# Kernel optimization log

Hardware: AMD Instinct MI355X
Metric: run time of the kernel (lower is better)

## Reference

```python
import jax, jax.numpy as jnp
import numpy as np

T, H, F, E, K = 1024, 2048, 1024, 8, 2  # tokens, hidden, intermediate, experts, top_k
RENORMALIZE = True


def setup_inputs() -> dict:
    key = jax.random.key(0)
    k1, k2, k3, k4, k5 = jax.random.split(key, 5)
    hidden_states = jax.random.normal(k1, (T, H), dtype=jnp.float32)
    router_logits = jax.random.normal(k2, (T, E), dtype=jnp.float32)
    w1 = jax.random.normal(k3, (E, H, F), dtype=jnp.float32) * 0.02  # gate proj
    w3 = jax.random.normal(k4, (E, H, F), dtype=jnp.float32) * 0.02  # up proj
    w2 = jax.random.normal(k5, (E, F, H), dtype=jnp.float32) * 0.02  # down proj
    return {"hidden_states": hidden_states, "router_logits": router_logits,
            "w1": w1, "w3": w3, "w2": w2}


def _moe_forward(x, router_logits, w1, w3, w2):
    # Top-K routing: softmax over all experts, select top-k, optional renormalize.
    probs = jax.nn.softmax(router_logits, axis=-1)            # [T, E]
    topk_vals, topk_ids = jax.lax.top_k(probs, K)             # [T, K]
    if RENORMALIZE:
        topk_vals = topk_vals / jnp.sum(topk_vals, axis=-1, keepdims=True)
    # Dense combine weights: zero for non-selected experts.   [T, E]
    tok_idx = jnp.arange(x.shape[0])[:, None]
    combine = jnp.zeros(probs.shape, dtype=x.dtype).at[tok_idx, topk_ids].set(topk_vals)
    # Expert SwiGLU FFN computed per expert over all tokens, masked-combined.
    g = jnp.einsum('th,ehf->etf', x, w1)                      # gate  [E, T, F]
    u = jnp.einsum('th,ehf->etf', x, w3)                      # up    [E, T, F]
    a = jax.nn.silu(g) * u                                    # silu activation
    y = jnp.einsum('etf,efh->eth', a, w2)                     # down  [E, T, H]
    out = jnp.einsum('eth,te->th', y, combine)                # weighted combine
    return out


def reference(hidden_states, router_logits, w1, w3, w2):
    return _moe_forward(hidden_states, router_logits, w1, w3, w2)
```

## Files before the change

kernel.cpp:

```cpp
#include <hip/hip_runtime.h>
#include <cstdint>
#include <cstddef>

#define T_TOK 1024
#define H_DIM 2048
#define F_DIM 1024
#define E_EXP 8
#define BM 64
#define BK 64
#define MAX_TILES 40
#define ROWCAP 2560

#define I_NTILES 25
#define I_TILE_E 32
#define I_TILE_R0 80
#define I_ROWTOK 4224
#define I_ROWW   6784
#define B_XB     37888
#define B_AWS    (B_XB + T_TOK*H_DIM*2)
#define B_W1T    (B_AWS + ROWCAP*F_DIM*2)
#define B_W3T    (B_W1T + E_EXP*F_DIM*H_DIM*2)
#define B_W2T    (B_W3T + E_EXP*F_DIM*H_DIM*2)

typedef __bf16 bf16x8 __attribute__((ext_vector_type(8)));
typedef float  f32x4  __attribute__((ext_vector_type(4)));

#define MFMA(a,b,c) __builtin_amdgcn_mfma_f32_16x16x32_bf16(a,b,c,0,0,0)

__device__ __forceinline__ void gload16(const void* g, void* l) {
  __builtin_amdgcn_global_load_lds(
      (const __attribute__((address_space(1))) void*)g,
      (__attribute__((address_space(3))) void*)l, 16, 0, 0);
}

__global__ __launch_bounds__(1024) void k_route(const float* __restrict__ logits,
                                                int* __restrict__ ws_i) {
  __shared__ int cnt[E_EXP], cur[E_EXP], offs_s[E_EXP];
  const int t = threadIdx.x;
  float* ws_f = (float*)ws_i;
  if (t < E_EXP) { cnt[t] = 0; cur[t] = 0; }
  __syncthreads();
  float l[E_EXP];
#pragma unroll
  for (int e = 0; e < E_EXP; ++e) l[e] = logits[t * E_EXP + e];
  int b0 = 0; float v0 = l[0];
#pragma unroll
  for (int e = 1; e < E_EXP; ++e) if (l[e] > v0) { v0 = l[e]; b0 = e; }
  int b1 = -1; float v1 = -3.4e38f;
#pragma unroll
  for (int e = 0; e < E_EXP; ++e) if (e != b0 && l[e] > v1) { v1 = l[e]; b1 = e; }
  float w0 = 1.f / (1.f + __expf(v1 - v0));
  float w1 = 1.f - w0;
  atomicAdd(&cnt[b0], 1);
  atomicAdd(&cnt[b1], 1);
  __syncthreads();
  if (t == 0) {
    int off = 0, nt = 0;
    for (int e = 0; e < E_EXP; ++e) {
      offs_s[e] = off;
      int ntile = (cnt[e] + BM - 1) / BM;
      for (int i = 0; i < ntile; ++i) {
        ws_i[I_TILE_E + nt] = e;
        ws_i[I_TILE_R0 + nt] = off + i * BM;
        ++nt;
      }
      off += ntile * BM;
    }
    ws_i[I_NTILES] = nt;
  }
  for (int i = t; i < ROWCAP; i += 1024) ws_i[I_ROWTOK + i] = -1;
  __syncthreads();
  {
    int p = atomicAdd(&cur[b0], 1);
    int s = offs_s[b0] + p;
    ws_i[I_ROWTOK + s] = t;
    ws_f[I_ROWW + s] = w0;
  }
  {
    int p = atomicAdd(&cur[b1], 1);
    int s = offs_s[b1] + p;
    ws_i[I_ROWTOK + s] = t;
    ws_f[I_ROWW + s] = w1;
  }
}

__global__ __launch_bounds__(256) void k_cvt(const float* __restrict__ x,
                                             __bf16* __restrict__ xb) {
  long i = (long)(blockIdx.x * 256 + threadIdx.x) * 8;
  float4 a = *(const float4*)(x + i);
  float4 b = *(const float4*)(x + i + 4);
  bf16x8 v;
  v[0] = (__bf16)a.x; v[1] = (__bf16)a.y; v[2] = (__bf16)a.z; v[3] = (__bf16)a.w;
  v[4] = (__bf16)b.x; v[5] = (__bf16)b.y; v[6] = (__bf16)b.z; v[7] = (__bf16)b.w;
  *(bf16x8*)(xb + i) = v;
}

__global__ __launch_bounds__(256) void k_cvtW(const float* __restrict__ w1,
                                              const float* __restrict__ w3,
                                              const float* __restrict__ w2,
                                              __bf16* __restrict__ w1t,
                                              __bf16* __restrict__ w3t,
                                              __bf16* __restrict__ w2t) {
  __shared__ __bf16 tr[64][66];
  const int z = blockIdx.z;
  const float* src; __bf16* dst; int R, C;
  if (z < 8)       { src = w1 + (size_t)z * H_DIM * F_DIM;        dst = w1t + (size_t)z * F_DIM * H_DIM;        R = H_DIM; C = F_DIM; }
  else if (z < 16) { src = w3 + (size_t)(z - 8) * H_DIM * F_DIM;  dst = w3t + (size_t)(z - 8) * F_DIM * H_DIM;  R = H_DIM; C = F_DIM; }
  else             { src = w2 + (size_t)(z - 16) * F_DIM * H_DIM; dst = w2t + (size_t)(z - 16) * H_DIM * F_DIM; R = F_DIM; C = H_DIM; }
  const int ti = blockIdx.x * 16 + blockIdx.y;
  const int nC = C >> 6;
  const int r0 = (ti / nC) * 64, c0 = (ti % nC) * 64;
  const float* s = src + (size_t)r0 * C + c0;
  __bf16* d = dst + (size_t)c0 * R + r0;
  const int t = threadIdx.x;
  const int lr = t >> 4, lc = (t & 15) * 4;
#pragma unroll
  for (int i = 0; i < 4; ++i) {
    int r = lr + i * 16;
    float4 f = *(const float4*)(s + (size_t)r * C + lc);
    tr[lc + 0][r] = (__bf16)f.x;
    tr[lc + 1][r] = (__bf16)f.y;
    tr[lc + 2][r] = (__bf16)f.z;
    tr[lc + 3][r] = (__bf16)f.w;
  }
  __syncthreads();
  const int oc = t >> 2, ok = (t & 3) * 16;
  *(bf16x8*)(d + (size_t)oc * R + ok)     = *(const bf16x8*)&tr[oc][ok];
  *(bf16x8*)(d + (size_t)oc * R + ok + 8) = *(const bf16x8*)&tr[oc][ok + 8];
}

__global__ __launch_bounds__(256) void k_gemm1(const __bf16* __restrict__ xb,
                                               const __bf16* __restrict__ w1t,
                                               const __bf16* __restrict__ w3t,
                                               const int* __restrict__ ws_i,
                                               __bf16* __restrict__ aws) {
  __shared__ __bf16 sm[2][3 * 4096];
  __shared__ int s_tok[BM];
  const int p = blockIdx.x;
  const int lg = (p & 7) * 80 + (p >> 3);
  const int tile = lg % MAX_TILES;
  const int n0 = (lg / MAX_TILES) * 64;
  if (tile >= ws_i[I_NTILES]) return;
  const int e  = ws_i[I_TILE_E + tile];
  const int r0 = ws_i[I_TILE_R0 + tile];
  const int tid = threadIdx.x, lane = tid & 63, wid = tid >> 6;
  const int wm = wid >> 1, wn = wid & 1;
  const int l15 = lane & 15, l4 = lane >> 4;
  if (tid < BM) {
    int tk = ws_i[I_ROWTOK + r0 + tid];
    s_tok[tid] = tk < 0 ? 0 : tk;
  }
  __syncthreads();
  const int rj0 = wid * 16 + (lane >> 3);
  const int rj1 = rj0 + 8;
  const int ks = ((lane & 7) ^ (lane >> 3)) * 8;
  const __bf16* gA0 = xb + (size_t)s_tok[rj0] * H_DIM + ks;
  const __bf16* gA1 = xb + (size_t)s_tok[rj1] * H_DIM + ks;
  const __bf16* w1e = w1t + (size_t)e * F_DIM * H_DIM;
  const __bf16* w3e = w3t + (size_t)e * F_DIM * H_DIM;
  const __bf16* gB1_0 = w1e + (size_t)(n0 + rj0) * H_DIM + ks;
  const __bf16* gB1_1 = w1e + (size_t)(n0 + rj1) * H_DIM + ks;
  const __bf16* gB3_0 = w3e + (size_t)(n0 + rj0) * H_DIM + ks;
  const __bf16* gB3_1 = w3e + (size_t)(n0 + rj1) * H_DIM + ks;
  const int c0 = wid * 2 * 512, c1 = c0 + 512;

  auto STAGE = [&](int b, int k0) {
    __bf16* As = &sm[b][0];
    __bf16* B1 = &sm[b][4096];
    __bf16* B3 = &sm[b][8192];
    gload16(gA0 + k0,   As + c0);
    gload16(gA1 + k0,   As + c1);
    gload16(gB1_0 + k0, B1 + c0);
    gload16(gB1_1 + k0, B1 + c1);
    gload16(gB3_0 + k0, B3 + c0);
    gload16(gB3_1 + k0, B3 + c1);
  };

  f32x4 accg[2][2] = {}; f32x4 accu[2][2] = {};
  auto COMPUTE = [&](int b) {
    const __bf16* As = &sm[b][0];
    const __bf16* B1 = &sm[b][4096];
    const __bf16* B3 = &sm[b][8192];
    __builtin_amdgcn_s_setprio(1);
#pragma unroll
    for (int kk = 0; kk < 2; ++kk) {
      const int sx = ((kk * 4 + l4) ^ (lane & 7)) << 3;
      const int ra0 = wm * 32 + l15, ra1 = ra0 + 16;
      const int rb0 = wn * 32 + l15, rb1 = rb0 + 16;
      bf16x8 a0  = *(const bf16x8*)&As[ra0 * 64 + sx];
      bf16x8 a1  = *(const bf16x8*)&As[ra1 * 64 + sx];
      bf16x8 b10 = *(const bf16x8*)&B1[rb0 * 64 + sx];
      bf16x8 b11 = *(const bf16x8*)&B1[rb1 * 64 + sx];
      bf16x8 b30 = *(const bf16x8*)&B3[rb0 * 64 + sx];
      bf16x8 b31 = *(const bf16x8*)&B3[rb1 * 64 + sx];
      accg[0][0] = MFMA(a0, b10, accg[0][0]);
      accg[0][1] = MFMA(a0, b11, accg[0][1]);
      accg[1][0] = MFMA(a1, b10, accg[1][0]);
      accg[1][1] = MFMA(a1, b11, accg[1][1]);
      accu[0][0] = MFMA(a0, b30, accu[0][0]);
      accu[0][1] = MFMA(a0, b31, accu[0][1]);
      accu[1][0] = MFMA(a1, b30, accu[1][0]);
      accu[1][1] = MFMA(a1, b31, accu[1][1]);
    }
    __builtin_amdgcn_s_setprio(0);
  };

  STAGE(0, 0);
  __syncthreads();
  int curb = 0;
  for (int t = 0; t < H_DIM / BK; ++t) {
    if (t + 1 < H_DIM / BK) STAGE(curb ^ 1, (t + 1) * BK);
    COMPUTE(curb);
    __syncthreads();
    curb ^= 1;
  }
#pragma unroll
  for (int fm = 0; fm < 2; ++fm)
#pragma unroll
    for (int fn = 0; fn < 2; ++fn)
#pragma unroll
      for (int r = 0; r < 4; ++r) {
        float g = accg[fm][fn][r], u = accu[fm][fn][r];
        float a = g / (1.f + __expf(-g)) * u;
        int row = r0 + wm * 32 + fm * 16 + l4 * 4 + r;
        int col = n0 + wn * 32 + fn * 16 + l15;
        aws[(size_t)row * F_DIM + col] = (__bf16)a;
      }
}

__global__ __launch_bounds__(256) void k_gemm2(const __bf16* __restrict__ aws,
                                               const __bf16* __restrict__ w2t,
                                               const int* __restrict__ ws_i,
                                               float* __restrict__ out) {
  __shared__ __bf16 sm[2][2 * 4096];
  __shared__ int s_tok[BM];
  __shared__ float s_w[BM];
  const int p = blockIdx.x;
  const int lg = (p & 7) * 160 + (p >> 3);
  const int tile = lg % MAX_TILES;
  const int h0 = (lg / MAX_TILES) * 64;
  if (tile >= ws_i[I_NTILES]) return;
  const int e  = ws_i[I_TILE_E + tile];
  const int r0 = ws_i[I_TILE_R0 + tile];
  const int tid = threadIdx.x, lane = tid & 63, wid = tid >> 6;
  const int wm = wid >> 1, wn = wid & 1;
  const int l15 = lane & 15, l4 = lane >> 4;
  const float* ws_f = (const float*)ws_i;
  if (tid < BM) {
    s_tok[tid] = ws_i[I_ROWTOK + r0 + tid];
    s_w[tid]   = ws_f[I_ROWW + r0 + tid];
  }
  __syncthreads();
  const int rj0 = wid * 16 + (lane >> 3);
  const int rj1 = rj0 + 8;
  const int ks = ((lane & 7) ^ (lane >> 3)) * 8;
  const __bf16* gA0 = aws + (size_t)(r0 + rj0) * F_DIM + ks;
  const __bf16* gA1 = aws + (size_t)(r0 + rj1) * F_DIM + ks;
  const __bf16* w2e = w2t + (size_t)e * H_DIM * F_DIM;
  const __bf16* gB0 = w2e + (size_t)(h0 + rj0) * F_DIM + ks;
  const __bf16* gB1 = w2e + (size_t)(h0 + rj1) * F_DIM + ks;
  const int c0 = wid * 2 * 512, c1 = c0 + 512;

  auto STAGE = [&](int b, int k0) {
    __bf16* As = &sm[b][0];
    __bf16* Bs = &sm[b][4096];
    gload16(gA0 + k0, As + c0);
    gload16(gA1 + k0, As + c1);
    gload16(gB0 + k0, Bs + c0);
    gload16(gB1 + k0, Bs + c1);
  };

  f32x4 acc[2][2] = {};
  auto COMPUTE = [&](int b) {
    const __bf16* As = &sm[b][0];
    const __bf16* Bs = &sm[b][4096];
    __builtin_amdgcn_s_setprio(1);
#pragma unroll
    for (int kk = 0; kk < 2; ++kk) {
      const int sx = ((kk * 4 + l4) ^ (lane & 7)) << 3;
      const int ra0 = wm * 32 + l15, ra1 = ra0 + 16;
      const int rb0 = wn * 32 + l15, rb1 = rb0 + 16;
      bf16x8 a0 = *(const bf16x8*)&As[ra0 * 64 + sx];
      bf16x8 a1 = *(const bf16x8*)&As[ra1 * 64 + sx];
      bf16x8 b0 = *(const bf16x8*)&Bs[rb0 * 64 + sx];
      bf16x8 b1 = *(const bf16x8*)&Bs[rb1 * 64 + sx];
      acc[0][0] = MFMA(a0, b0, acc[0][0]);
      acc[0][1] = MFMA(a0, b1, acc[0][1]);
      acc[1][0] = MFMA(a1, b0, acc[1][0]);
      acc[1][1] = MFMA(a1, b1, acc[1][1]);
    }
    __builtin_amdgcn_s_setprio(0);
  };

  STAGE(0, 0);
  __syncthreads();
  int curb = 0;
  for (int t = 0; t < F_DIM / BK; ++t) {
    if (t + 1 < F_DIM / BK) STAGE(curb ^ 1, (t + 1) * BK);
    COMPUTE(curb);
    __syncthreads();
    curb ^= 1;
  }
#pragma unroll
  for (int fm = 0; fm < 2; ++fm)
#pragma unroll
    for (int fn = 0; fn < 2; ++fn)
#pragma unroll
      for (int r = 0; r < 4; ++r) {
        int lrow = wm * 32 + fm * 16 + l4 * 4 + r;
        int t = s_tok[lrow];
        if (t >= 0) {
          float v = acc[fm][fn][r] * s_w[lrow];
          atomicAdd(out + (size_t)t * H_DIM + h0 + wn * 32 + fn * 16 + l15, v);
        }
      }
}

extern "C" void kernel_launch(void* const* d_in, const int* in_sizes, int n_in,
                              void* d_out, int out_size, void* d_ws, size_t ws_size,
                              hipStream_t stream) {
  (void)in_sizes; (void)n_in; (void)out_size; (void)ws_size;
  const float* x      = (const float*)d_in[0];
  const float* logits = (const float*)d_in[1];
  const float* w1     = (const float*)d_in[2];
  const float* w3     = (const float*)d_in[3];
  const float* w2     = (const float*)d_in[4];
  float* out = (float*)d_out;
  int* ws_i = (int*)d_ws;
  __bf16* xb  = (__bf16*)((char*)d_ws + B_XB);
  __bf16* aws = (__bf16*)((char*)d_ws + B_AWS);
  __bf16* w1t = (__bf16*)((char*)d_ws + B_W1T);
  __bf16* w3t = (__bf16*)((char*)d_ws + B_W3T);
  __bf16* w2t = (__bf16*)((char*)d_ws + B_W2T);

  hipMemsetAsync(d_out, 0, (size_t)T_TOK * H_DIM * sizeof(float), stream);
  k_route<<<1, 1024, 0, stream>>>(logits, ws_i);
  k_cvt<<<dim3(T_TOK * H_DIM / (256 * 8)), 256, 0, stream>>>(x, xb);
  k_cvtW<<<dim3(32, 16, 24), 256, 0, stream>>>(w1, w3, w2, w1t, w3t, w2t);
  k_gemm1<<<dim3(MAX_TILES * (F_DIM / 64)), 256, 0, stream>>>(xb, w1t, w3t, ws_i, aws);
  k_gemm2<<<dim3(MAX_TILES * (H_DIM / 64)), 256, 0, stream>>>(aws, w2t, ws_i, out);
}
```

Baseline: 132.9 us.

## Fuse fp32 weight conversion and transpose into the expert GEMM loaders

Drops the separate pass that converts and transposes all expert weights to bf16. Each GEMM now reads fp32 weight tiles straight into registers, converts and transposes them in registers, and writes them to padded shared memory. The register prefetch runs two stages ahead. This avoids writing and re-reading the bf16 weight copies, but each weight tile is now read in fp32 by every token-tile block that uses it, which doubles the bytes per reuse and adds conversion work inside the main loop.

```diff
diff --git a/kernel.cpp b/kernel.cpp
--- a/kernel.cpp
+++ b/kernel.cpp
@@ -8,6 +8,7 @@
 #define E_EXP 8
 #define BM 64
 #define BK 64
+#define SP 72
 #define MAX_TILES 40
 #define ROWCAP 2560
 
@@ -18,11 +19,9 @@
 #define I_ROWW   6784
 #define B_XB     37888
 #define B_AWS    (B_XB + T_TOK*H_DIM*2)
-#define B_W1T    (B_AWS + ROWCAP*F_DIM*2)
-#define B_W3T    (B_W1T + E_EXP*F_DIM*H_DIM*2)
-#define B_W2T    (B_W3T + E_EXP*F_DIM*H_DIM*2)
 
 typedef __bf16 bf16x8 __attribute__((ext_vector_type(8)));
+typedef __bf16 bf16x4 __attribute__((ext_vector_type(4)));
 typedef float  f32x4  __attribute__((ext_vector_type(4)));
 
 #define MFMA(a,b,c) __builtin_amdgcn_mfma_f32_16x16x32_bf16(a,b,c,0,0,0)
@@ -95,46 +94,14 @@
   *(bf16x8*)(xb + i) = v;
 }
 
-__global__ __launch_bounds__(256) void k_cvtW(const float* __restrict__ w1,
-                                              const float* __restrict__ w3,
-                                              const float* __restrict__ w2,
-                                              __bf16* __restrict__ w1t,
-                                              __bf16* __restrict__ w3t,
-                                              __bf16* __restrict__ w2t) {
-  __shared__ __bf16 tr[64][66];
-  const int z = blockIdx.z;
-  const float* src; __bf16* dst; int R, C;
-  if (z < 8)       { src = w1 + (size_t)z * H_DIM * F_DIM;        dst = w1t + (size_t)z * F_DIM * H_DIM;        R = H_DIM; C = F_DIM; }
-  else if (z < 16) { src = w3 + (size_t)(z - 8) * H_DIM * F_DIM;  dst = w3t + (size_t)(z - 8) * F_DIM * H_DIM;  R = H_DIM; C = F_DIM; }
-  else             { src = w2 + (size_t)(z - 16) * F_DIM * H_DIM; dst = w2t + (size_t)(z - 16) * H_DIM * F_DIM; R = F_DIM; C = H_DIM; }
-  const int ti = blockIdx.x * 16 + blockIdx.y;
-  const int nC = C >> 6;
-  const int r0 = (ti / nC) * 64, c0 = (ti % nC) * 64;
-  const float* s = src + (size_t)r0 * C + c0;
-  __bf16* d = dst + (size_t)c0 * R + r0;
-  const int t = threadIdx.x;
-  const int lr = t >> 4, lc = (t & 15) * 4;
-#pragma unroll
-  for (int i = 0; i < 4; ++i) {
-    int r = lr + i * 16;
-    float4 f = *(const float4*)(s + (size_t)r * C + lc);
-    tr[lc + 0][r] = (__bf16)f.x;
-    tr[lc + 1][r] = (__bf16)f.y;
-    tr[lc + 2][r] = (__bf16)f.z;
-    tr[lc + 3][r] = (__bf16)f.w;
-  }
-  __syncthreads();
-  const int oc = t >> 2, ok = (t & 3) * 16;
-  *(bf16x8*)(d + (size_t)oc * R + ok)     = *(const bf16x8*)&tr[oc][ok];
-  *(bf16x8*)(d + (size_t)oc * R + ok + 8) = *(const bf16x8*)&tr[oc][ok + 8];
-}
-
 __global__ __launch_bounds__(256) void k_gemm1(const __bf16* __restrict__ xb,
-                                               const __bf16* __restrict__ w1t,
-                                               const __bf16* __restrict__ w3t,
+                                               const float* __restrict__ w1,
+                                               const float* __restrict__ w3,
                                                const int* __restrict__ ws_i,
                                                __bf16* __restrict__ aws) {
-  __shared__ __bf16 sm[2][3 * 4096];
+  __shared__ __bf16 Asm[2][4096];
+  __shared__ __bf16 B1s[2][64][SP];
+  __shared__ __bf16 B3s[2][64][SP];
   __shared__ int s_tok[BM];
   const int p = blockIdx.x;
   const int lg = (p & 7) * 80 + (p >> 3);
@@ -145,7 +112,8 @@
   const int r0 = ws_i[I_TILE_R0 + tile];
   const int tid = threadIdx.x, lane = tid & 63, wid = tid >> 6;
   const int wm = wid >> 1, wn = wid & 1;
-  const int l15 = lane & 15, l4 = lane >> 4;
+  const int l15 = lane & 15, l4 = lane >> 4, lk8 = (lane >> 4) << 3;
+  const int nb = (tid & 15) * 4, kq = (tid >> 4) * 4;
   if (tid < BM) {
     int tk = ws_i[I_ROWTOK + r0 + tid];
     s_tok[tid] = tk < 0 ? 0 : tk;
@@ -156,43 +124,49 @@
   const int ks = ((lane & 7) ^ (lane >> 3)) * 8;
   const __bf16* gA0 = xb + (size_t)s_tok[rj0] * H_DIM + ks;
   const __bf16* gA1 = xb + (size_t)s_tok[rj1] * H_DIM + ks;
-  const __bf16* w1e = w1t + (size_t)e * F_DIM * H_DIM;
-  const __bf16* w3e = w3t + (size_t)e * F_DIM * H_DIM;
-  const __bf16* gB1_0 = w1e + (size_t)(n0 + rj0) * H_DIM + ks;
-  const __bf16* gB1_1 = w1e + (size_t)(n0 + rj1) * H_DIM + ks;
-  const __bf16* gB3_0 = w3e + (size_t)(n0 + rj0) * H_DIM + ks;
-  const __bf16* gB3_1 = w3e + (size_t)(n0 + rj1) * H_DIM + ks;
   const int c0 = wid * 2 * 512, c1 = c0 + 512;
-
-  auto STAGE = [&](int b, int k0) {
-    __bf16* As = &sm[b][0];
-    __bf16* B1 = &sm[b][4096];
-    __bf16* B3 = &sm[b][8192];
-    gload16(gA0 + k0,   As + c0);
-    gload16(gA1 + k0,   As + c1);
-    gload16(gB1_0 + k0, B1 + c0);
-    gload16(gB1_1 + k0, B1 + c1);
-    gload16(gB3_0 + k0, B3 + c0);
-    gload16(gB3_1 + k0, B3 + c1);
+  const float* pB1 = w1 + (size_t)e * H_DIM * F_DIM + n0 + nb;
+  const float* pB3 = w3 + (size_t)e * H_DIM * F_DIM + n0 + nb;
+
+  f32x4 qa1[4], qa3[4], qb1[4], qb3[4];
+
+  auto STAGEA = [&](int b, int t) {
+    gload16(gA0 + t * BK, &Asm[b][c0]);
+    gload16(gA1 + t * BK, &Asm[b][c1]);
+  };
+  auto LOADR = [&](f32x4 (&q1)[4], f32x4 (&q3)[4], int t) {
+    const int k0 = t * BK + kq;
+#pragma unroll
+    for (int j = 0; j < 4; ++j) {
+      q1[j] = *(const f32x4*)(pB1 + (size_t)(k0 + j) * F_DIM);
+      q3[j] = *(const f32x4*)(pB3 + (size_t)(k0 + j) * F_DIM);
+    }
+  };
+  auto WRITEB = [&](int b, f32x4 (&q1)[4], f32x4 (&q3)[4]) {
+#pragma unroll
+    for (int u = 0; u < 4; ++u) {
+      bf16x4 v1, v3;
+#pragma unroll
+      for (int j = 0; j < 4; ++j) { v1[j] = (__bf16)q1[j][u]; v3[j] = (__bf16)q3[j][u]; }
+      *(bf16x4*)&B1s[b][nb + u][kq] = v1;
+      *(bf16x4*)&B3s[b][nb + u][kq] = v3;
+    }
   };
 
   f32x4 accg[2][2] = {}; f32x4 accu[2][2] = {};
   auto COMPUTE = [&](int b) {
-    const __bf16* As = &sm[b][0];
-    const __bf16* B1 = &sm[b][4096];
-    const __bf16* B3 = &sm[b][8192];
+    const __bf16* As = &Asm[b][0];
     __builtin_amdgcn_s_setprio(1);
 #pragma unroll
     for (int kk = 0; kk < 2; ++kk) {
       const int sx = ((kk * 4 + l4) ^ (lane & 7)) << 3;
-      const int ra0 = wm * 32 + l15, ra1 = ra0 + 16;
-      const int rb0 = wn * 32 + l15, rb1 = rb0 + 16;
-      bf16x8 a0  = *(const bf16x8*)&As[ra0 * 64 + sx];
-      bf16x8 a1  = *(const bf16x8*)&As[ra1 * 64 + sx];
-      bf16x8 b10 = *(const bf16x8*)&B1[rb0 * 64 + sx];
-      bf16x8 b11 = *(const bf16x8*)&B1[rb1 * 64 + sx];
-      bf16x8 b30 = *(const bf16x8*)&B3[rb0 * 64 + sx];
-      bf16x8 b31 = *(const bf16x8*)&B3[rb1 * 64 + sx];
+      const int kb = kk * 32 + lk8;
+      bf16x8 a0  = *(const bf16x8*)&As[(wm * 32 + l15) * 64 + sx];
+      bf16x8 a1  = *(const bf16x8*)&As[(wm * 32 + 16 + l15) * 64 + sx];
+      bf16x8 b10 = *(const bf16x8*)&B1s[b][wn * 32 + l15][kb];
+      bf16x8 b11 = *(const bf16x8*)&B1s[b][wn * 32 + 16 + l15][kb];
+      bf16x8 b30 = *(const bf16x8*)&B3s[b][wn * 32 + l15][kb];
+      bf16x8 b31 = *(const bf16x8*)&B3s[b][wn * 32 + 16 + l15][kb];
       accg[0][0] = MFMA(a0, b10, accg[0][0]);
       accg[0][1] = MFMA(a0, b11, accg[0][1]);
       accg[1][0] = MFMA(a1, b10, accg[1][0]);
@@ -205,14 +179,22 @@
     __builtin_amdgcn_s_setprio(0);
   };
 
-  STAGE(0, 0);
-  __syncthreads();
-  int curb = 0;
-  for (int t = 0; t < H_DIM / BK; ++t) {
-    if (t + 1 < H_DIM / BK) STAGE(curb ^ 1, (t + 1) * BK);
-    COMPUTE(curb);
+  const int NT = H_DIM / BK;
+  LOADR(qa1, qa3, 0);
+  LOADR(qb1, qb3, 1);
+  STAGEA(0, 0);
+  WRITEB(0, qa1, qa3);
+  LOADR(qa1, qa3, 2);
+  __syncthreads();
+  for (int t = 0; t < NT; t += 2) {
+    if (t + 1 < NT) { STAGEA(1, t + 1); WRITEB(1, qb1, qb3); }
+    if (t + 3 < NT) LOADR(qb1, qb3, t + 3);
+    COMPUTE(0);
     __syncthreads();
-    curb ^= 1;
+    if (t + 2 < NT) { STAGEA(0, t + 2); WRITEB(0, qa1, qa3); }
+    if (t + 4 < NT) LOADR(qa1, qa3, t + 4);
+    COMPUTE(1);
+    __syncthreads();
   }
 #pragma unroll
   for (int fm = 0; fm < 2; ++fm)
@@ -229,10 +211,11 @@
 }
 
 __global__ __launch_bounds__(256) void k_gemm2(const __bf16* __restrict__ aws,
-                                               const __bf16* __restrict__ w2t,
+                                               const float* __restrict__ w2,
                                                const int* __restrict__ ws_i,
                                                float* __restrict__ out) {
-  __shared__ __bf16 sm[2][2 * 4096];
+  __shared__ __bf16 Asm[2][4096];
+  __shared__ __bf16 Bs[2][64][SP];
   __shared__ int s_tok[BM];
   __shared__ float s_w[BM];
   const int p = blockIdx.x;
@@ -244,7 +227,8 @@
   const int r0 = ws_i[I_TILE_R0 + tile];
   const int tid = threadIdx.x, lane = tid & 63, wid = tid >> 6;
   const int wm = wid >> 1, wn = wid & 1;
-  const int l15 = lane & 15, l4 = lane >> 4;
+  const int l15 = lane & 15, l4 = lane >> 4, lk8 = (lane >> 4) << 3;
+  const int nb = (tid & 15) * 4, kq = (tid >> 4) * 4;
   const float* ws_f = (const float*)ws_i;
   if (tid < BM) {
     s_tok[tid] = ws_i[I_ROWTOK + r0 + tid];
@@ -256,34 +240,43 @@
   const int ks = ((lane & 7) ^ (lane >> 3)) * 8;
   const __bf16* gA0 = aws + (size_t)(r0 + rj0) * F_DIM + ks;
   const __bf16* gA1 = aws + (size_t)(r0 + rj1) * F_DIM + ks;
-  const __bf16* w2e = w2t + (size_t)e * H_DIM * F_DIM;
-  const __bf16* gB0 = w2e + (size_t)(h0 + rj0) * F_DIM + ks;
-  const __bf16* gB1 = w2e + (size_t)(h0 + rj1) * F_DIM + ks;
   const int c0 = wid * 2 * 512, c1 = c0 + 512;
-
-  auto STAGE = [&](int b, int k0) {
-    __bf16* As = &sm[b][0];
-    __bf16* Bs = &sm[b][4096];
-    gload16(gA0 + k0, As + c0);
-    gload16(gA1 + k0, As + c1);
-    gload16(gB0 + k0, Bs + c0);
-    gload16(gB1 + k0, Bs + c1);
+  const float* pB2 = w2 + (size_t)e * F_DIM * H_DIM + h0 + nb;
+
+  f32x4 qa2[4], qb2[4];
+
+  auto STAGEA = [&](int b, int t) {
+    gload16(gA0 + t * BK, &Asm[b][c0]);
+    gload16(gA1 + t * BK, &Asm[b][c1]);
+  };
+  auto LOADR = [&](f32x4 (&q2)[4], int t) {
+    const int k0 = t * BK + kq;
+#pragma unroll
+    for (int j = 0; j < 4; ++j)
+      q2[j] = *(const f32x4*)(pB2 + (size_t)(k0 + j) * H_DIM);
+  };
+  auto WRITEB = [&](int b, f32x4 (&q2)[4]) {
+#pragma unroll
+    for (int u = 0; u < 4; ++u) {
+      bf16x4 v;
+#pragma unroll
+      for (int j = 0; j < 4; ++j) v[j] = (__bf16)q2[j][u];
+      *(bf16x4*)&Bs[b][nb + u][kq] = v;
+    }
   };
 
   f32x4 acc[2][2] = {};
   auto COMPUTE = [&](int b) {
-    const __bf16* As = &sm[b][0];
-    const __bf16* Bs = &sm[b][4096];
+    const __bf16* As = &Asm[b][0];
     __builtin_amdgcn_s_setprio(1);
 #pragma unroll
     for (int kk = 0; kk < 2; ++kk) {
       const int sx = ((kk * 4 + l4) ^ (lane & 7)) << 3;
-      const int ra0 = wm * 32 + l15, ra1 = ra0 + 16;
-      const int rb0 = wn * 32 + l15, rb1 = rb0 + 16;
-      bf16x8 a0 = *(const bf16x8*)&As[ra0 * 64 + sx];
-      bf16x8 a1 = *(const bf16x8*)&As[ra1 * 64 + sx];
-      bf16x8 b0 = *(const bf16x8*)&Bs[rb0 * 64 + sx];
-      bf16x8 b1 = *(const bf16x8*)&Bs[rb1 * 64 + sx];
+      const int kb = kk * 32 + lk8;
+      bf16x8 a0 = *(const bf16x8*)&As[(wm * 32 + l15) * 64 + sx];
+      bf16x8 a1 = *(const bf16x8*)&As[(wm * 32 + 16 + l15) * 64 + sx];
+      bf16x8 b0 = *(const bf16x8*)&Bs[b][wn * 32 + l15][kb];
+      bf16x8 b1 = *(const bf16x8*)&Bs[b][wn * 32 + 16 + l15][kb];
       acc[0][0] = MFMA(a0, b0, acc[0][0]);
       acc[0][1] = MFMA(a0, b1, acc[0][1]);
       acc[1][0] = MFMA(a1, b0, acc[1][0]);
@@ -292,14 +285,22 @@
     __builtin_amdgcn_s_setprio(0);
   };
 
-  STAGE(0, 0);
-  __syncthreads();
-  int curb = 0;
-  for (int t = 0; t < F_DIM / BK; ++t) {
-    if (t + 1 < F_DIM / BK) STAGE(curb ^ 1, (t + 1) * BK);
-    COMPUTE(curb);
+  const int NT = F_DIM / BK;
+  LOADR(qa2, 0);
+  LOADR(qb2, 1);
+  STAGEA(0, 0);
+  WRITEB(0, qa2);
+  LOADR(qa2, 2);
+  __syncthreads();
+  for (int t = 0; t < NT; t += 2) {
+    if (t + 1 < NT) { STAGEA(1, t + 1); WRITEB(1, qb2); }
+    if (t + 3 < NT) LOADR(qb2, t + 3);
+    COMPUTE(0);
     __syncthreads();
-    curb ^= 1;
+    if (t + 2 < NT) { STAGEA(0, t + 2); WRITEB(0, qa2); }
+    if (t + 4 < NT) LOADR(qa2, t + 4);
+    COMPUTE(1);
+    __syncthreads();
   }
 #pragma unroll
   for (int fm = 0; fm < 2; ++fm)
@@ -329,14 +330,10 @@
   int* ws_i = (int*)d_ws;
   __bf16* xb  = (__bf16*)((char*)d_ws + B_XB);
   __bf16* aws = (__bf16*)((char*)d_ws + B_AWS);
-  __bf16* w1t = (__bf16*)((char*)d_ws + B_W1T);
-  __bf16* w3t = (__bf16*)((char*)d_ws + B_W3T);
-  __bf16* w2t = (__bf16*)((char*)d_ws + B_W2T);
 
   hipMemsetAsync(d_out, 0, (size_t)T_TOK * H_DIM * sizeof(float), stream);
   k_route<<<1, 1024, 0, stream>>>(logits, ws_i);
   k_cvt<<<dim3(T_TOK * H_DIM / (256 * 8)), 256, 0, stream>>>(x, xb);
-  k_cvtW<<<dim3(32, 16, 24), 256, 0, stream>>>(w1, w3, w2, w1t, w3t, w2t);
-  k_gemm1<<<dim3(MAX_TILES * (F_DIM / 64)), 256, 0, stream>>>(xb, w1t, w3t, ws_i, aws);
-  k_gemm2<<<dim3(MAX_TILES * (H_DIM / 64)), 256, 0, stream>>>(aws, w2t, ws_i, out);
-}
+  k_gemm1<<<dim3(MAX_TILES * (F_DIM / 64)), 256, 0, stream>>>(xb, w1, w3, ws_i, aws);
+  k_gemm2<<<dim3(MAX_TILES * (H_DIM / 64)), 256, 0, stream>>>(aws, w2, ws_i, out);
+}
```

After: 144.3 us. 8.6% more time.
